# Kernel optimization log

Measured on AMD Instinct MI355X. Metric: run time of the kernel, lower is better.

## Reference

```python
import jax, jax.numpy as jnp
import numpy as np

N = 100000   # nodes
E = 1600000  # edges (avg degree 16)
D = 128      # in_features == out_features (required by residual branch)


def setup_inputs() -> dict:
    key = jax.random.key(0)
    ks = jax.random.split(key, 8)
    return {
        "x": jax.random.normal(ks[0], (N, D), dtype=jnp.float32),
        "W": jax.random.normal(ks[1], (D, D), dtype=jnp.float32) * (1.0 / np.sqrt(D)),
        "b": jax.random.normal(ks[2], (D,), dtype=jnp.float32) * 0.01,
        "Wres": jax.random.normal(ks[3], (D, D), dtype=jnp.float32) * (1.0 / np.sqrt(D)),
        "bres": jax.random.normal(ks[4], (D,), dtype=jnp.float32) * 0.01,
        "edge_val": jax.random.uniform(ks[5], (E,), dtype=jnp.float32),
        "edge_row": jax.random.randint(ks[6], (E,), 0, N, dtype=jnp.int32),
        "edge_col": jax.random.randint(ks[7], (E,), 0, N, dtype=jnp.int32),
    }


def reference(x, W, b, Wres, bres, edge_val, edge_row, edge_col):
    # Dense projection: [N, D]
    h = x @ W + b
    # Sparse adjacency SpMM: out[i] = sum_{e: row[e]==i} val[e] * h[col[e]]
    msgs = edge_val[:, None] * h[edge_col]            # [E, D] gather
    agg = jax.ops.segment_sum(msgs, edge_row, num_segments=N)  # [N, D] scatter-add
    # Activation (relu), then residual Linear applied to post-activation tensor
    # (faithful to the torch code: x = act(x); x = x + residual(x)).
    a = jax.nn.relu(agg)
    out = a + (a @ Wres + bres)
    # dropout = 0.0 -> identity (eval mode)
    return out
```

## Files before the change

### kernel.cpp

```cpp
#include <hip/hip_runtime.h>
#include <hip/hip_bf16.h>

#define D 128
#define RCH 128
#define NCH 782
#define NCHP 1024
#define NB_S 500
#define CH_S 3200
#define OS2 800
#define CAP 3072
#define PB 128
#define GB64 1563

typedef __attribute__((ext_vector_type(8))) short short8v;
typedef __attribute__((ext_vector_type(4))) float float4v;

__device__ inline ushort f2bf(float f) {
    __hip_bfloat16 h = __float2bfloat16(f);
    return __builtin_bit_cast(ushort, h);
}
__device__ inline float bf2f(ushort u) {
    return __builtin_bit_cast(float, (uint)u << 16);
}
__device__ inline ushort relu_bf(ushort u) { return (u & 0x8000u) ? (ushort)0 : u; }

__device__ inline void stage_wt_lds(char* smem, const ushort* __restrict__ Wt,
                                    int tid) {
#pragma unroll
    for (int i = 0; i < 8; ++i) {
        const int L = tid * 128 + i * 16;
        const int row = L >> 8;
        const int off = L & 255;
        *(short8v*)(smem + row * 256 + (off ^ ((row & 7) << 4))) =
            *(const short8v*)((const char*)Wt + L);
    }
}

__device__ inline void stage_wt_lds512(char* smem, const ushort* __restrict__ Wt,
                                       int tid) {
#pragma unroll
    for (int i = 0; i < 4; ++i) {
        const int L = tid * 64 + i * 16;
        const int row = L >> 8;
        const int off = L & 255;
        *(short8v*)(smem + row * 256 + (off ^ ((row & 7) << 4))) =
            *(const short8v*)((const char*)Wt + L);
    }
}

__global__ __launch_bounds__(256) void k0_prep(const float* __restrict__ W,
                                               const float* __restrict__ Wres,
                                               ushort* __restrict__ Wt,
                                               ushort* __restrict__ Wtres) {
    const int flat = blockIdx.x * 256 + threadIdx.x;
    const float* src = (flat < 16384) ? W : Wres;
    ushort* dst = (flat < 16384) ? Wt : Wtres;
    const int f = flat & 16383;
    const int k = f >> 7, c = f & 127;
    dst[c * D + k] = f2bf(src[f]);
}

__global__ __launch_bounds__(256) void kA_scatter_gemm(
    const float* __restrict__ ev, const int* __restrict__ er,
    const int* __restrict__ ec, int* __restrict__ offs2,
    int2* __restrict__ tmp, int E,
    const float* __restrict__ X, const ushort* __restrict__ Wt,
    const float* __restrict__ bias, ushort* __restrict__ hb, int N) {
    __shared__ char smem[32768];

    if (blockIdx.x < NB_S) {
        int* h = (int*)smem;
        int* sscan = (int*)(smem + 4 * NCHP);
        const int b = blockIdx.x;
        const int t = threadIdx.x;
        const int start = b * CH_S;
        const int end = min(E, start + CH_S);
        const int nfull = (end - start) & ~3;

        for (int k = t; k < NCHP; k += 256) h[k] = 0;
        __syncthreads();

        for (int o = 4 * t; o < nfull; o += 1024) {
            const int4 r4 = *(const int4*)(er + start + o);
            atomicAdd(&h[r4.x >> 7], 1);
            atomicAdd(&h[r4.y >> 7], 1);
            atomicAdd(&h[r4.z >> 7], 1);
            atomicAdd(&h[r4.w >> 7], 1);
        }
        for (int o = nfull + t; o < end - start; o += 256)
            atomicAdd(&h[er[start + o] >> 7], 1);
        __syncthreads();

        const int a0 = h[4 * t], a1 = h[4 * t + 1];
        const int a2 = h[4 * t + 2], a3 = h[4 * t + 3];
        const int tsum = a0 + a1 + a2 + a3;
        sscan[t] = tsum;
        __syncthreads();
        for (int o = 1; o < 256; o <<= 1) {
            const int a = (t >= o) ? sscan[t - o] : 0;
            __syncthreads();
            sscan[t] += a;
            __syncthreads();
        }
        const int ex = start + sscan[t] - tsum;
        const int c0 = 4 * t;
        h[c0]     = ex;
        h[c0 + 1] = ex + a0;
        h[c0 + 2] = ex + a0 + a1;
        h[c0 + 3] = ex + a0 + a1 + a2;
        int* od = offs2 + (long)b * OS2;
#pragma unroll
        for (int i = 0; i < 4; ++i)
            if (c0 + i <= NCH) od[c0 + i] = h[c0 + i];
        __syncthreads();

        for (int o = 4 * t; o < nfull; o += 1024) {
            const int4 r4 = *(const int4*)(er + start + o);
            const int4 c4 = *(const int4*)(ec + start + o);
            const float4 v4 = *(const float4*)(ev + start + o);
            const int p0 = atomicAdd(&h[r4.x >> 7], 1);
            const int p1 = atomicAdd(&h[r4.y >> 7], 1);
            const int p2 = atomicAdd(&h[r4.z >> 7], 1);
            const int p3 = atomicAdd(&h[r4.w >> 7], 1);
            tmp[p0] = make_int2((c4.x << 7) | (r4.x & 127), __float_as_int(v4.x));
            tmp[p1] = make_int2((c4.y << 7) | (r4.y & 127), __float_as_int(v4.y));
            tmp[p2] = make_int2((c4.z << 7) | (r4.z & 127), __float_as_int(v4.z));
            tmp[p3] = make_int2((c4.w << 7) | (r4.w & 127), __float_as_int(v4.w));
        }
        for (int o = nfull + t; o < end - start; o += 256) {
            const int e = start + o;
            const int r = er[e];
            const int pos = atomicAdd(&h[r >> 7], 1);
            tmp[pos] = make_int2((ec[e] << 7) | (r & 127), __float_as_int(ev[e]));
        }
        return;
    }

    const int g = blockIdx.x - NB_S;
    const int t = threadIdx.x;
    const int lane = t & 63;
    const int w = t >> 6;
    const int l16 = lane & 15;
    const int lk = lane >> 4;
    const long wRow = (long)g * 64 + w * 16;

    short8v afrag[4];
    {
        long r = wRow + l16;
        if (r >= N) r = N - 1;
        const float* xp = X + r * D + lk * 8;
#pragma unroll
        for (int ks = 0; ks < 4; ++ks) {
            const float4 u0 = *(const float4*)(xp + ks * 32);
            const float4 u1 = *(const float4*)(xp + ks * 32 + 4);
            float f[8] = {u0.x, u0.y, u0.z, u0.w, u1.x, u1.y, u1.z, u1.w};
            short8v a;
#pragma unroll
            for (int i = 0; i < 8; ++i) a[i] = (short)f2bf(f[i]);
            afrag[ks] = a;
        }
    }

    stage_wt_lds(smem, Wt, t);
    __syncthreads();

    float4v acc[8];
#pragma unroll
    for (int q = 0; q < 8; ++q) acc[q] = (float4v)(0.0f);

    const int swz = (l16 & 7) << 4;
#pragma unroll
    for (int ks = 0; ks < 4; ++ks) {
#pragma unroll
        for (int q = 0; q < 8; ++q) {
            const int row = q * 16 + l16;
            const short8v bfrag = *(const short8v*)(
                smem + row * 256 + ((ks * 64 + lk * 16) ^ swz));
            acc[q] = __builtin_amdgcn_mfma_f32_16x16x32_bf16(afrag[ks], bfrag,
                                                             acc[q], 0, 0, 0);
        }
    }

#pragma unroll
    for (int q = 0; q < 8; ++q) {
        const int col = q * 16 + l16;
        const float bb = bias[col];
#pragma unroll
        for (int i = 0; i < 4; ++i) {
            const long row = wRow + lk * 4 + i;
            if (row < N) hb[row * D + col] = f2bf(acc[q][i] + bb);
        }
    }
}

__global__ __launch_bounds__(256) void kB_sort(const int2* __restrict__ tmp,
                                               const int* __restrict__ offs2,
                                               int2* __restrict__ recs,
                                               int* __restrict__ rowptr) {
    __shared__ int2 buf[CAP];
    __shared__ int sb[256];
    __shared__ int hcnt[RCH];
    __shared__ int sc[RCH];
    __shared__ int cur[RCH];
    const int c = blockIdx.x;
    const int t = threadIdx.x;
    const int s = c * CAP;

    int segA = 0, cbA = 0, segB = 0, cbB = 0;
    if (t < NB_S / 2) {
        const int* oA = offs2 + (long)(2 * t) * OS2;
        const int* oB = offs2 + (long)(2 * t + 1) * OS2;
        segA = oA[c]; cbA = oA[c + 1] - segA;
        segB = oB[c]; cbB = oB[c + 1] - segB;
    }
    const int cb = cbA + cbB;

    sb[t] = cb;
    __syncthreads();
    for (int o = 1; o < 256; o <<= 1) {
        const int a = (t >= o) ? sb[t - o] : 0;
        __syncthreads();
        sb[t] += a;
        __syncthreads();
    }
    const int base = sb[t] - cb;
    const int cnt = min(sb[255], CAP);

    if (t < RCH) hcnt[t] = 0;
    __syncthreads();

    for (int i = 0; i < cbA; ++i) {
        const int p = base + i;
        if (p >= CAP) break;
        const int2 r = tmp[segA + i];
        buf[p] = r;
        atomicAdd(&hcnt[r.x & 127], 1);
    }
    for (int i = 0; i < cbB; ++i) {
        const int p = base + cbA + i;
        if (p >= CAP) break;
        const int2 r = tmp[segB + i];
        buf[p] = r;
        atomicAdd(&hcnt[r.x & 127], 1);
    }
    __syncthreads();

    if (t < RCH) sc[t] = hcnt[t];
    __syncthreads();
    for (int o = 1; o < RCH; o <<= 1) {
        const int a = (t < RCH && t >= o) ? sc[t - o] : 0;
        __syncthreads();
        if (t < RCH) sc[t] += a;
        __syncthreads();
    }
    if (t < RCH) {
        const int ex = s + sc[t] - hcnt[t];
        cur[t] = ex;
        rowptr[c * (RCH + 1) + t] = ex;
    }
    if (t == 0) rowptr[c * (RCH + 1) + RCH] = s + cnt;
    __syncthreads();

    for (int k = t; k < cnt; k += 256) {
        const int2 r = buf[k];
        const int pos = atomicAdd(&cur[r.x & 127], 1);
        recs[pos] = make_int2((r.x >> 7) << 8, r.y);
    }
}

#define GFMA2(accv, rr, gg)                                                   \
    accv.x = fmaf(__int_as_float((rr).y), bf2f((ushort)((gg)&0xffffu)), accv.x);\
    accv.y = fmaf(__int_as_float((rr).y), bf2f((ushort)((gg) >> 16)), accv.y);

__device__ inline void drain_row(const int2* __restrict__ recs,
                                 const char* __restrict__ hpc,
                                 int& j, int e, float2& acc) {
    for (; j + 8 <= e; j += 8) {
        const int2 r0 = recs[j],     r1 = recs[j + 1];
        const int2 r2 = recs[j + 2], r3 = recs[j + 3];
        const int2 r4 = recs[j + 4], r5 = recs[j + 5];
        const int2 r6 = recs[j + 6], r7 = recs[j + 7];
        const uint g0 = *(const uint*)(hpc + (uint)r0.x);
        const uint g1 = *(const uint*)(hpc + (uint)r1.x);
        const uint g2 = *(const uint*)(hpc + (uint)r2.x);
        const uint g3 = *(const uint*)(hpc + (uint)r3.x);
        const uint g4 = *(const uint*)(hpc + (uint)r4.x);
        const uint g5 = *(const uint*)(hpc + (uint)r5.x);
        const uint g6 = *(const uint*)(hpc + (uint)r6.x);
        const uint g7 = *(const uint*)(hpc + (uint)r7.x);
        GFMA2(acc, r0, g0) GFMA2(acc, r1, g1) GFMA2(acc, r2, g2) GFMA2(acc, r3, g3)
        GFMA2(acc, r4, g4) GFMA2(acc, r5, g5) GFMA2(acc, r6, g6) GFMA2(acc, r7, g7)
    }
    for (; j + 2 <= e; j += 2) {
        const int2 r0 = recs[j], r1 = recs[j + 1];
        const uint g0 = *(const uint*)(hpc + (uint)r0.x);
        const uint g1 = *(const uint*)(hpc + (uint)r1.x);
        GFMA2(acc, r0, g0) GFMA2(acc, r1, g1)
    }
    if (j < e) {
        const int2 r0 = recs[j];
        const uint g0 = *(const uint*)(hpc + (uint)r0.x);
        GFMA2(acc, r0, g0)
    }
}

__global__ __launch_bounds__(512, 8) void k56_spmm_gemm1(
    const ushort* __restrict__ hb, const int2* __restrict__ recs,
    const int* __restrict__ rowptr, const ushort* __restrict__ Wtres,
    const float* __restrict__ bres, float* __restrict__ Y, int N) {
    __shared__ char wsm[32768];
    __shared__ char agg[4096];
    const int t = threadIdx.x;
    const int w = t >> 6;
    const int lane = t & 63;

    stage_wt_lds512(wsm, Wtres, t);

    const int rowA = blockIdx.x * 16 + w * 2;
    const int c = rowA >> 7;
    const int tr = rowA & 127;
    int rp = 0;
    if (lane < 3) rp = rowptr[c * (RCH + 1) + tr + lane];
    const int sA = __shfl(rp, 0);
    const int eA = __shfl(rp, 1);
    const int sB = eA;
    const int eB = __shfl(rp, 2);

    const char* hpc = (const char*)hb + lane * 4;
    float2 accA = make_float2(0.f, 0.f);
    float2 accB = make_float2(0.f, 0.f);

    int jA = sA, jB = sB;
    while (jA + 8 <= eA && jB + 8 <= eB) {
        const int2 a0 = recs[jA],     a1 = recs[jA + 1];
        const int2 a2 = recs[jA + 2], a3 = recs[jA + 3];
        const int2 a4 = recs[jA + 4], a5 = recs[jA + 5];
        const int2 a6 = recs[jA + 6], a7 = recs[jA + 7];
        const int2 b0 = recs[jB],     b1 = recs[jB + 1];
        const int2 b2 = recs[jB + 2], b3 = recs[jB + 3];
        const int2 b4 = recs[jB + 4], b5 = recs[jB + 5];
        const int2 b6 = recs[jB + 6], b7 = recs[jB + 7];
        const uint ga0 = *(const uint*)(hpc + (uint)a0.x);
        const uint ga1 = *(const uint*)(hpc + (uint)a1.x);
        const uint ga2 = *(const uint*)(hpc + (uint)a2.x);
        const uint ga3 = *(const uint*)(hpc + (uint)a3.x);
        const uint ga4 = *(const uint*)(hpc + (uint)a4.x);
        const uint ga5 = *(const uint*)(hpc + (uint)a5.x);
        const uint ga6 = *(const uint*)(hpc + (uint)a6.x);
        const uint ga7 = *(const uint*)(hpc + (uint)a7.x);
        const uint gb0 = *(const uint*)(hpc + (uint)b0.x);
        const uint gb1 = *(const uint*)(hpc + (uint)b1.x);
        const uint gb2 = *(const uint*)(hpc + (uint)b2.x);
        const uint gb3 = *(const uint*)(hpc + (uint)b3.x);
        const uint gb4 = *(const uint*)(hpc + (uint)b4.x);
        const uint gb5 = *(const uint*)(hpc + (uint)b5.x);
        const uint gb6 = *(const uint*)(hpc + (uint)b6.x);
        const uint gb7 = *(const uint*)(hpc + (uint)b7.x);
        GFMA2(accA, a0, ga0) GFMA2(accA, a1, ga1) GFMA2(accA, a2, ga2) GFMA2(accA, a3, ga3)
        GFMA2(accA, a4, ga4) GFMA2(accA, a5, ga5) GFMA2(accA, a6, ga6) GFMA2(accA, a7, ga7)
        GFMA2(accB, b0, gb0) GFMA2(accB, b1, gb1) GFMA2(accB, b2, gb2) GFMA2(accB, b3, gb3)
        GFMA2(accB, b4, gb4) GFMA2(accB, b5, gb5) GFMA2(accB, b6, gb6) GFMA2(accB, b7, gb7)
        jA += 8;
        jB += 8;
    }
    drain_row(recs, hpc, jA, eA, accA);
    drain_row(recs, hpc, jB, eB, accB);

    {
        const uint pA = (uint)relu_bf(f2bf(accA.x)) |
                        ((uint)relu_bf(f2bf(accA.y)) << 16);
        const uint pB = (uint)relu_bf(f2bf(accB.x)) |
                        ((uint)relu_bf(f2bf(accB.y)) << 16);
        const int rA = 2 * w, rB = 2 * w + 1;
        *(uint*)(agg + rA * 256 + ((lane * 4) ^ ((rA & 7) << 4))) = pA;
        *(uint*)(agg + rB * 256 + ((lane * 4) ^ ((rB & 7) << 4))) = pB;
    }
    __syncthreads();

    const int l16 = lane & 15;
    const int lk = lane >> 4;
    const int ct = w;
    const int aswz = (l16 & 7) << 4;

    float4v acc = (float4v)(0.0f);
#pragma unroll
    for (int ks = 0; ks < 4; ++ks) {
        const short8v af = *(const short8v*)(
            agg + l16 * 256 + ((ks * 64 + lk * 16) ^ aswz));
        const short8v bf = *(const short8v*)(
            wsm + (ct * 16 + l16) * 256 + ((ks * 64 + lk * 16) ^ aswz));
        acc = __builtin_amdgcn_mfma_f32_16x16x32_bf16(af, bf, acc, 0, 0, 0);
    }

    const int col = ct * 16 + l16;
    const float bb = bres[col];
#pragma unroll
    for (int i = 0; i < 4; ++i) {
        const int rl = lk * 4 + i;
        const ushort au = *(const ushort*)(
            agg + rl * 256 + ((col * 2) ^ ((rl & 7) << 4)));
        const long grow = (long)blockIdx.x * 16 + rl;
        Y[grow * D + col] = bf2f(au) + acc[i] + bb;
    }
}

extern "C" void kernel_launch(void* const* d_in, const int* in_sizes, int n_in,
                              void* d_out, int out_size, void* d_ws, size_t ws_size,
                              hipStream_t stream) {
    const float* x    = (const float*)d_in[0];
    const float* W    = (const float*)d_in[1];
    const float* b    = (const float*)d_in[2];
    const float* Wres = (const float*)d_in[3];
    const float* bres = (const float*)d_in[4];
    const float* ev   = (const float*)d_in[5];
    const int*   er   = (const int*)d_in[6];
    const int*   ec   = (const int*)d_in[7];

    float* out = (float*)d_out;

    const int n = in_sizes[0] / D;
    const int e = in_sizes[5];

    char* ws = (char*)d_ws;
    size_t off_b = 0;
    auto alloc = [&](size_t bytes) {
        void* p = ws + off_b;
        off_b += (bytes + 511) & ~size_t(511);
        return p;
    };
    ushort* hb     = (ushort*)alloc((size_t)n * D * sizeof(ushort));
    int2*   recs   = (int2*)alloc((size_t)NCH * CAP * sizeof(int2));
    int*    rowptr = (int*)alloc((size_t)NCH * (RCH + 1) * sizeof(int));
    ushort* Wt     = (ushort*)alloc((size_t)D * D * sizeof(ushort));
    ushort* Wtres  = (ushort*)alloc((size_t)D * D * sizeof(ushort));
    int2*   tmp    = (int2*)alloc((size_t)NB_S * CH_S * sizeof(int2));
    int*    offs2  = (int*)alloc((size_t)NB_S * OS2 * sizeof(int));
    (void)ws_size;

    k0_prep<<<PB, 256, 0, stream>>>(W, Wres, Wt, Wtres);

    kA_scatter_gemm<<<NB_S + GB64, 256, 0, stream>>>(ev, er, ec, offs2, tmp, e,
                                                     x, Wt, b, hb, n);

    kB_sort<<<NCH, 256, 0, stream>>>(tmp, offs2, recs, rowptr);

    k56_spmm_gemm1<<<(n + 15) / 16, 512, 0, stream>>>(hb, recs, rowptr,
                                                      Wtres, bres, out, n);
}
```

Baseline: 142.6 us.

## Make residual GEMM per-wave to drop block-wide barrier after SpMM

```diff
diff --git a/kernel.cpp b/kernel.cpp
--- a/kernel.cpp
+++ b/kernel.cpp
@@ -309,12 +309,13 @@
     const int* __restrict__ rowptr, const ushort* __restrict__ Wtres,
     const float* __restrict__ bres, float* __restrict__ Y, int N) {
     __shared__ char wsm[32768];
-    __shared__ char agg[4096];
+    __shared__ char slot[8][512];
     const int t = threadIdx.x;
     const int w = t >> 6;
     const int lane = t & 63;
 
     stage_wt_lds512(wsm, Wtres, t);
+    __syncthreads();
 
     const int rowA = blockIdx.x * 16 + w * 2;
     const int c = rowA >> 7;
@@ -371,36 +372,52 @@
                         ((uint)relu_bf(f2bf(accA.y)) << 16);
         const uint pB = (uint)relu_bf(f2bf(accB.x)) |
                         ((uint)relu_bf(f2bf(accB.y)) << 16);
-        const int rA = 2 * w, rB = 2 * w + 1;
-        *(uint*)(agg + rA * 256 + ((lane * 4) ^ ((rA & 7) << 4))) = pA;
-        *(uint*)(agg + rB * 256 + ((lane * 4) ^ ((rB & 7) << 4))) = pB;
-    }
-    __syncthreads();
+        *(uint*)(slot[w] + lane * 4) = pA;
+        *(uint*)(slot[w] + 256 + lane * 4) = pB;
+    }
+    asm volatile("s_waitcnt lgkmcnt(0)" ::: "memory");
+    __builtin_amdgcn_sched_barrier(0);
 
     const int l16 = lane & 15;
     const int lk = lane >> 4;
-    const int ct = w;
-    const int aswz = (l16 & 7) << 4;
-
-    float4v acc = (float4v)(0.0f);
-#pragma unroll
-    for (int ks = 0; ks < 4; ++ks) {
-        const short8v af = *(const short8v*)(
-            agg + l16 * 256 + ((ks * 64 + lk * 16) ^ aswz));
-        const short8v bf = *(const short8v*)(
-            wsm + (ct * 16 + l16) * 256 + ((ks * 64 + lk * 16) ^ aswz));
-        acc = __builtin_amdgcn_mfma_f32_16x16x32_bf16(af, bf, acc, 0, 0, 0);
-    }
-
-    const int col = ct * 16 + l16;
-    const float bb = bres[col];
-#pragma unroll
-    for (int i = 0; i < 4; ++i) {
-        const int rl = lk * 4 + i;
-        const ushort au = *(const ushort*)(
-            agg + rl * 256 + ((col * 2) ^ ((rl & 7) << 4)));
-        const long grow = (long)blockIdx.x * 16 + rl;
-        Y[grow * D + col] = bf2f(au) + acc[i] + bb;
+    const int arow = l16 & 1;
+
+    short8v afrag[4];
+#pragma unroll
+    for (int ks = 0; ks < 4; ++ks)
+        afrag[ks] = *(const short8v*)(slot[w] + arow * 256 + ks * 64 + lk * 16);
+
+    const int swz = (l16 & 7) << 4;
+    const long rowY = (long)rowA;
+
+#pragma unroll
+    for (int half = 0; half < 2; ++half) {
+        float4v acc[4];
+#pragma unroll
+        for (int q = 0; q < 4; ++q) acc[q] = (float4v)(0.0f);
+#pragma unroll
+        for (int ks = 0; ks < 4; ++ks) {
+#pragma unroll
+            for (int q = 0; q < 4; ++q) {
+                const int ct = half * 4 + q;
+                const short8v bfrag = *(const short8v*)(
+                    wsm + (ct * 16 + l16) * 256 + ((ks * 64 + lk * 16) ^ swz));
+                acc[q] = __builtin_amdgcn_mfma_f32_16x16x32_bf16(
+                    afrag[ks], bfrag, acc[q], 0, 0, 0);
+            }
+        }
+        if (lk == 0) {
+#pragma unroll
+            for (int q = 0; q < 4; ++q) {
+                const int ct = half * 4 + q;
+                const int col = ct * 16 + l16;
+                const float bb = bres[col];
+                const float a0 = bf2f(*(const ushort*)(slot[w] + col * 2));
+                const float a1 = bf2f(*(const ushort*)(slot[w] + 256 + col * 2));
+                Y[rowY * D + col] = a0 + acc[q][0] + bb;
+                Y[(rowY + 1) * D + col] = a1 + acc[q][1] + bb;
+            }
+        }
     }
 }
 
```

Result: slower. 151.2 us (+6.1%).

## Process 64 rows per block with LDS work queue and direct-global Wres fragments

Applied to the files above, without the earlier changes.

```diff
diff --git a/kernel.cpp b/kernel.cpp
--- a/kernel.cpp
+++ b/kernel.cpp
@@ -29,18 +29,6 @@
 #pragma unroll
     for (int i = 0; i < 8; ++i) {
         const int L = tid * 128 + i * 16;
-        const int row = L >> 8;
-        const int off = L & 255;
-        *(short8v*)(smem + row * 256 + (off ^ ((row & 7) << 4))) =
-            *(const short8v*)((const char*)Wt + L);
-    }
-}
-
-__device__ inline void stage_wt_lds512(char* smem, const ushort* __restrict__ Wt,
-                                       int tid) {
-#pragma unroll
-    for (int i = 0; i < 4; ++i) {
-        const int L = tid * 64 + i * 16;
         const int row = L >> 8;
         const int off = L & 255;
         *(short8v*)(smem + row * 256 + (off ^ ((row & 7) << 4))) =
@@ -308,99 +296,119 @@
     const ushort* __restrict__ hb, const int2* __restrict__ recs,
     const int* __restrict__ rowptr, const ushort* __restrict__ Wtres,
     const float* __restrict__ bres, float* __restrict__ Y, int N) {
-    __shared__ char wsm[32768];
-    __shared__ char agg[4096];
+    __shared__ char agg[64 * 256];
+    __shared__ int qcur;
     const int t = threadIdx.x;
-    const int w = t >> 6;
     const int lane = t & 63;
 
-    stage_wt_lds512(wsm, Wtres, t);
-
-    const int rowA = blockIdx.x * 16 + w * 2;
-    const int c = rowA >> 7;
-    const int tr = rowA & 127;
-    int rp = 0;
-    if (lane < 3) rp = rowptr[c * (RCH + 1) + tr + lane];
-    const int sA = __shfl(rp, 0);
-    const int eA = __shfl(rp, 1);
-    const int sB = eA;
-    const int eB = __shfl(rp, 2);
+    if (t == 0) qcur = 0;
+    __syncthreads();
 
     const char* hpc = (const char*)hb + lane * 4;
-    float2 accA = make_float2(0.f, 0.f);
-    float2 accB = make_float2(0.f, 0.f);
-
-    int jA = sA, jB = sB;
-    while (jA + 8 <= eA && jB + 8 <= eB) {
-        const int2 a0 = recs[jA],     a1 = recs[jA + 1];
-        const int2 a2 = recs[jA + 2], a3 = recs[jA + 3];
-        const int2 a4 = recs[jA + 4], a5 = recs[jA + 5];
-        const int2 a6 = recs[jA + 6], a7 = recs[jA + 7];
-        const int2 b0 = recs[jB],     b1 = recs[jB + 1];
-        const int2 b2 = recs[jB + 2], b3 = recs[jB + 3];
-        const int2 b4 = recs[jB + 4], b5 = recs[jB + 5];
-        const int2 b6 = recs[jB + 6], b7 = recs[jB + 7];
-        const uint ga0 = *(const uint*)(hpc + (uint)a0.x);
-        const uint ga1 = *(const uint*)(hpc + (uint)a1.x);
-        const uint ga2 = *(const uint*)(hpc + (uint)a2.x);
-        const uint ga3 = *(const uint*)(hpc + (uint)a3.x);
-        const uint ga4 = *(const uint*)(hpc + (uint)a4.x);
-        const uint ga5 = *(const uint*)(hpc + (uint)a5.x);
-        const uint ga6 = *(const uint*)(hpc + (uint)a6.x);
-        const uint ga7 = *(const uint*)(hpc + (uint)a7.x);
-        const uint gb0 = *(const uint*)(hpc + (uint)b0.x);
-        const uint gb1 = *(const uint*)(hpc + (uint)b1.x);
-        const uint gb2 = *(const uint*)(hpc + (uint)b2.x);
-        const uint gb3 = *(const uint*)(hpc + (uint)b3.x);
-        const uint gb4 = *(const uint*)(hpc + (uint)b4.x);
-        const uint gb5 = *(const uint*)(hpc + (uint)b5.x);
-        const uint gb6 = *(const uint*)(hpc + (uint)b6.x);
-        const uint gb7 = *(const uint*)(hpc + (uint)b7.x);
-        GFMA2(accA, a0, ga0) GFMA2(accA, a1, ga1) GFMA2(accA, a2, ga2) GFMA2(accA, a3, ga3)
-        GFMA2(accA, a4, ga4) GFMA2(accA, a5, ga5) GFMA2(accA, a6, ga6) GFMA2(accA, a7, ga7)
-        GFMA2(accB, b0, gb0) GFMA2(accB, b1, gb1) GFMA2(accB, b2, gb2) GFMA2(accB, b3, gb3)
-        GFMA2(accB, b4, gb4) GFMA2(accB, b5, gb5) GFMA2(accB, b6, gb6) GFMA2(accB, b7, gb7)
-        jA += 8;
-        jB += 8;
-    }
-    drain_row(recs, hpc, jA, eA, accA);
-    drain_row(recs, hpc, jB, eB, accB);
-
-    {
+    const long rowBase = (long)blockIdx.x * 64;
+
+    for (;;) {
+        int p;
+        if (lane == 0) p = atomicAdd(&qcur, 1);
+        p = __shfl(p, 0);
+        if (p >= 32) break;
+
+        const int rowA = (int)rowBase + p * 2;
+        const int c = rowA >> 7;
+        const int tr = rowA & 127;
+        int rp = 0;
+        if (lane < 3) rp = rowptr[c * (RCH + 1) + tr + lane];
+        const int sA = __shfl(rp, 0);
+        const int eA = __shfl(rp, 1);
+        const int sB = eA;
+        const int eB = __shfl(rp, 2);
+
+        float2 accA = make_float2(0.f, 0.f);
+        float2 accB = make_float2(0.f, 0.f);
+
+        int jA = sA, jB = sB;
+        while (jA + 8 <= eA && jB + 8 <= eB) {
+            const int2 a0 = recs[jA],     a1 = recs[jA + 1];
+            const int2 a2 = recs[jA + 2], a3 = recs[jA + 3];
+            const int2 a4 = recs[jA + 4], a5 = recs[jA + 5];
+            const int2 a6 = recs[jA + 6], a7 = recs[jA + 7];
+            const int2 b0 = recs[jB],     b1 = recs[jB + 1];
+            const int2 b2 = recs[jB + 2], b3 = recs[jB + 3];
+            const int2 b4 = recs[jB + 4], b5 = recs[jB + 5];
+            const int2 b6 = recs[jB + 6], b7 = recs[jB + 7];
+            const uint ga0 = *(const uint*)(hpc + (uint)a0.x);
+            const uint ga1 = *(const uint*)(hpc + (uint)a1.x);
+            const uint ga2 = *(const uint*)(hpc + (uint)a2.x);
+            const uint ga3 = *(const uint*)(hpc + (uint)a3.x);
+            const uint ga4 = *(const uint*)(hpc + (uint)a4.x);
+            const uint ga5 = *(const uint*)(hpc + (uint)a5.x);
+            const uint ga6 = *(const uint*)(hpc + (uint)a6.x);
+            const uint ga7 = *(const uint*)(hpc + (uint)a7.x);
+            const uint gb0 = *(const uint*)(hpc + (uint)b0.x);
+            const uint gb1 = *(const uint*)(hpc + (uint)b1.x);
+            const uint gb2 = *(const uint*)(hpc + (uint)b2.x);
+            const uint gb3 = *(const uint*)(hpc + (uint)b3.x);
+            const uint gb4 = *(const uint*)(hpc + (uint)b4.x);
+            const uint gb5 = *(const uint*)(hpc + (uint)b5.x);
+            const uint gb6 = *(const uint*)(hpc + (uint)b6.x);
+            const uint gb7 = *(const uint*)(hpc + (uint)b7.x);
+            GFMA2(accA, a0, ga0) GFMA2(accA, a1, ga1) GFMA2(accA, a2, ga2) GFMA2(accA, a3, ga3)
+            GFMA2(accA, a4, ga4) GFMA2(accA, a5, ga5) GFMA2(accA, a6, ga6) GFMA2(accA, a7, ga7)
+            GFMA2(accB, b0, gb0) GFMA2(accB, b1, gb1) GFMA2(accB, b2, gb2) GFMA2(accB, b3, gb3)
+            GFMA2(accB, b4, gb4) GFMA2(accB, b5, gb5) GFMA2(accB, b6, gb6) GFMA2(accB, b7, gb7)
+            jA += 8;
+            jB += 8;
+        }
+        drain_row(recs, hpc, jA, eA, accA);
+        drain_row(recs, hpc, jB, eB, accB);
+
         const uint pA = (uint)relu_bf(f2bf(accA.x)) |
                         ((uint)relu_bf(f2bf(accA.y)) << 16);
         const uint pB = (uint)relu_bf(f2bf(accB.x)) |
                         ((uint)relu_bf(f2bf(accB.y)) << 16);
-        const int rA = 2 * w, rB = 2 * w + 1;
+        const int rA = 2 * p, rB = 2 * p + 1;
         *(uint*)(agg + rA * 256 + ((lane * 4) ^ ((rA & 7) << 4))) = pA;
         *(uint*)(agg + rB * 256 + ((lane * 4) ^ ((rB & 7) << 4))) = pB;
     }
     __syncthreads();
 
+    const int w = t >> 6;
     const int l16 = lane & 15;
     const int lk = lane >> 4;
     const int ct = w;
     const int aswz = (l16 & 7) << 4;
 
-    float4v acc = (float4v)(0.0f);
+    float4v acc[4];
+#pragma unroll
+    for (int rt = 0; rt < 4; ++rt) acc[rt] = (float4v)(0.0f);
+
 #pragma unroll
     for (int ks = 0; ks < 4; ++ks) {
-        const short8v af = *(const short8v*)(
-            agg + l16 * 256 + ((ks * 64 + lk * 16) ^ aswz));
-        const short8v bf = *(const short8v*)(
-            wsm + (ct * 16 + l16) * 256 + ((ks * 64 + lk * 16) ^ aswz));
-        acc = __builtin_amdgcn_mfma_f32_16x16x32_bf16(af, bf, acc, 0, 0, 0);
+        const short8v bfrag = *(const short8v*)(
+            Wtres + (long)(ct * 16 + l16) * D + ks * 32 + lk * 8);
+#pragma unroll
+        for (int rt = 0; rt < 4; ++rt) {
+            const short8v afrag = *(const short8v*)(
+                agg + (rt * 16 + l16) * 256 + ((ks * 64 + lk * 16) ^ aswz));
+            acc[rt] = __builtin_amdgcn_mfma_f32_16x16x32_bf16(
+                afrag, bfrag, acc[rt], 0, 0, 0);
+        }
     }
 
     const int col = ct * 16 + l16;
     const float bb = bres[col];
 #pragma unroll
-    for (int i = 0; i < 4; ++i) {
-        const int rl = lk * 4 + i;
-        const ushort au = *(const ushort*)(
-            agg + rl * 256 + ((col * 2) ^ ((rl & 7) << 4)));
-        const long grow = (long)blockIdx.x * 16 + rl;
-        Y[grow * D + col] = bf2f(au) + acc[i] + bb;
+    for (int rt = 0; rt < 4; ++rt) {
+#pragma unroll
+        for (int i = 0; i < 4; ++i) {
+            const int rl = rt * 16 + lk * 4 + i;
+            const long grow = rowBase + rl;
+            if (grow < N) {
+                const float a = bf2f(*(const ushort*)(
+                    agg + rl * 256 + ((col * 2) ^ ((rl & 7) << 4))));
+                Y[grow * D + col] = a + acc[rt][i] + bb;
+            }
+        }
     }
 }
 
@@ -444,6 +452,6 @@
 
     kB_sort<<<NCH, 256, 0, stream>>>(tmp, offs2, recs, rowptr);
 
-    k56_spmm_gemm1<<<(n + 15) / 16, 512, 0, stream>>>(hb, recs, rowptr,
+    k56_spmm_gemm1<<<(n + 63) / 64, 512, 0, stream>>>(hb, recs, rowptr,
                                                       Wtres, bres, out, n);
 }
```

Result: slower. 147.1 us (+3.2%).
